# Kernel optimization log

Measured on AMD Instinct MI355X. Metric: run time of the kernel, lower is better.

## Reference

```python
import jax, jax.numpy as jnp
import numpy as np

K = 2            # num_classes (fixed in module)
THRESH = 0.01    # CdistThreshold
MAX_ITERS = 3    # loop breaks when Ci > 3 -> at most 3 work iterations


def _l2norm(x, eps=1e-12):
    # torch F.normalize(dim=1) on [N, C]-style rows -> normalize last axis here
    n = jnp.linalg.norm(x, axis=-1, keepdims=True)
    return x / jnp.maximum(n, eps)


def _step(feats, centers):
    """One k-means iteration, vectorized over batch.
    feats:   [B, N, C]  centers: [K, C]
    Returns (new_centers [K,C], CurDist scalar, labels [B,N])."""
    B = feats.shape[0]
    fn = _l2norm(feats)
    cn = _l2norm(centers)
    # cosine distance 0.5*(1 - cos_sim): [B, N, K]
    dists = 0.5 * (1.0 - jnp.einsum('bnc,kc->bnk', fn, cn))
    labels = jnp.argmin(dists, axis=-1)                      # [B, N]
    mask = jax.nn.one_hot(labels, K, dtype=feats.dtype)      # [B, N, K]
    sums = jnp.einsum('bnc,bnk->bkc', feats, mask)           # [B, K, C]
    counts = jnp.sum(mask, axis=1)                           # [B, K]
    centers_iter = sums / (counts[..., None] + 1.0)          # [B, K, C] (note +1 as in torch)
    # per-batch mean cosine similarity between new per-batch centers and old centers
    num = jnp.sum(centers_iter * centers[None], axis=-1)     # [B, K]
    den = jnp.maximum(
        jnp.linalg.norm(centers_iter, axis=-1) * jnp.linalg.norm(centers, axis=-1)[None],
        1e-8)
    cdist = jnp.mean(num / den, axis=-1)                     # [B]
    new_centers = jnp.sum(centers_iter, axis=0) / B          # centersIterout / B
    cur_dist = jnp.sum(cdist) / B                            # CdistT / B
    return new_centers, cur_dist, labels


def setup_inputs() -> dict:
    key = jax.random.key(0)
    k1, k2 = jax.random.split(key)
    FeatureT = jax.random.normal(k1, (8, 256, 256, 256), dtype=jnp.float32)
    centerInit = jax.random.normal(k2, (K, 256), dtype=jnp.float32)
    return {"FeatureT": FeatureT, "centerInit": centerInit}


def reference(FeatureT, centerInit):
    B, C = FeatureT.shape[0], FeatureT.shape[1]
    feats = FeatureT.reshape(B, C, -1).transpose(0, 2, 1)    # [B, N, C]
    # iteration 1 always runs (centers = centerInit)
    centers, cur_dist, labels = _step(feats, centerInit)
    done = cur_dist < THRESH
    # iterations 2..3, frozen once converged (matches the while-loop break)
    for _ in range(MAX_ITERS - 1):
        nc, cd, lb = _step(feats, centers)
        centers = jnp.where(done, centers, nc)
        labels = jnp.where(done, labels, lb)
        cur_dist = jnp.where(done, cur_dist, cd)
        done = done | (cur_dist < THRESH)
    labels_onehot = jax.nn.one_hot(labels.reshape(-1), K, dtype=jnp.float32)  # [B*N, K]
    # torch returns centersIterout.detach()
    return jax.lax.stop_gradient(centers), labels, labels_onehot, cur_dist
```

## Files before the change

### kernel.cpp

```cpp
#include <hip/hip_runtime.h>
#include <stdint.h>

#define CDIM   256
#define NPIX   65536
#define NBATCH 8
#define SLABS  64
#define SCOLS  1024
#define NBLOCKS (NBATCH * SLABS)
#define KTHRESH 0.01

#define WS_DELTA 0
#define WS_CENT  256
#define WS_T     768
#define WS_S1    2816
#define WS_CNT   4864
#define WS_DONE  4872

#define OUT_LABELS 512
#define OUT_ONEHOT (512 + NBATCH * NPIX)
#define OUT_CDIST  (512 + NBATCH * NPIX + 2 * NBATCH * NPIX)

__device__ __forceinline__ double block_reduce(double v, double* sh) {
  const int t = threadIdx.x;
  #pragma unroll
  for (int off = 32; off > 0; off >>= 1) v += __shfl_down(v, off, 64);
  __syncthreads();
  if ((t & 63) == 0) sh[t >> 6] = v;
  __syncthreads();
  return sh[0] + sh[1] + sh[2] + sh[3];
}

__device__ __forceinline__ void block_reduce4(double v[4], double* sh) {
  const int t = threadIdx.x;
  #pragma unroll
  for (int off = 32; off > 0; off >>= 1) {
    v[0] += __shfl_down(v[0], off, 64);
    v[1] += __shfl_down(v[1], off, 64);
    v[2] += __shfl_down(v[2], off, 64);
    v[3] += __shfl_down(v[3], off, 64);
  }
  __syncthreads();
  if ((t & 63) == 0) {
    const int w = t >> 6;
    sh[w] = v[0]; sh[4 + w] = v[1]; sh[8 + w] = v[2]; sh[12 + w] = v[3];
  }
  __syncthreads();
  #pragma unroll
  for (int k = 0; k < 4; ++k) v[k] = sh[4 * k] + sh[4 * k + 1] + sh[4 * k + 2] + sh[4 * k + 3];
}

__global__ __launch_bounds__(256) void init_kernel(const float* __restrict__ cinit,
                                                   float* __restrict__ ws) {
  __shared__ double sh[16];
  const int t = threadIdx.x;
  for (int i = t; i < NBATCH * CDIM; i += 256) { ws[WS_T + i] = 0.f; ws[WS_S1 + i] = 0.f; }
  if (t < NBATCH) ((unsigned int*)(ws + WS_CNT))[t] = 0u;
  if (t == 0) ((int*)(ws + WS_DONE))[0] = 0;
  const float c0f = cinit[t], c1f = cinit[CDIM + t];
  ws[WS_CENT + t] = c0f;
  ws[WS_CENT + CDIM + t] = c1f;
  const double c0 = (double)c0f, c1 = (double)c1f;
  double n0 = sqrt(block_reduce(c0 * c0, sh));
  double n1 = sqrt(block_reduce(c1 * c1, sh));
  n0 = fmax(n0, 1e-12); n1 = fmax(n1, 1e-12);
  ws[WS_DELTA + t] = (float)(c1 / n1) - (float)(c0 / n0);
}

__global__ __launch_bounds__(256) void pass_kernel(const float* __restrict__ F,
                                                   float* __restrict__ ws,
                                                   float* __restrict__ out,
                                                   int iter) {
  if (iter > 0 && ((const volatile int*)(ws + WS_DONE))[0] != 0) return;

  __shared__ double deltaD[CDIM];
  __shared__ float s1p[CDIM * 4];
  __shared__ float tp[CDIM * 4];
  __shared__ unsigned cntS;

  const int t = threadIdx.x;
  const int w = t >> 6;
  const int l = t & 63;
  const int b = blockIdx.x >> 6;
  const int n0 = (blockIdx.x & 63) * SCOLS;

  if (t < CDIM) deltaD[t] = (double)ws[WS_DELTA + t];
  if (t == 0) cntS = 0u;
  __syncthreads();

  const float4* __restrict__ Fv =
      (const float4*)(F + (size_t)b * CDIM * NPIX + n0);
  const int rstride = NPIX / 4;

  double d0 = 0.0, d1 = 0.0, d2 = 0.0, d3 = 0.0;
  #pragma unroll 16
  for (int c = 0; c < CDIM; ++c) {
    const float4 v = Fv[(size_t)c * rstride + t];
    const double dc = deltaD[c];
    d0 = fma(dc, (double)v.x, d0);
    d1 = fma(dc, (double)v.y, d1);
    d2 = fma(dc, (double)v.z, d2);
    d3 = fma(dc, (double)v.w, d3);
  }
  const float m0 = d0 > 0.0 ? 1.f : 0.f;
  const float m1 = d1 > 0.0 ? 1.f : 0.f;
  const float m2 = d2 > 0.0 ? 1.f : 0.f;
  const float m3 = d3 > 0.0 ? 1.f : 0.f;

  const int gi0 = b * NPIX + n0 + 4 * t;
  *(float4*)(out + OUT_LABELS + gi0) = make_float4(m0, m1, m2, m3);
  *(float4*)(out + OUT_ONEHOT + 2 * gi0)     = make_float4(1.f - m0, m0, 1.f - m1, m1);
  *(float4*)(out + OUT_ONEHOT + 2 * gi0 + 4) = make_float4(1.f - m2, m2, 1.f - m3, m3);

  const unsigned cw = (unsigned)(__popcll(__ballot(d0 > 0.0)) +
                                 __popcll(__ballot(d1 > 0.0)) +
                                 __popcll(__ballot(d2 > 0.0)) +
                                 __popcll(__ballot(d3 > 0.0)));
  if (l == 0) atomicAdd(&cntS, cw);

  const bool first = (iter == 0);
  #pragma unroll 8
  for (int c = CDIM - 1; c >= 0; --c) {
    const float4 v = Fv[(size_t)c * rstride + t];
    float s1 = 0.f;
    s1 = fmaf(m0, v.x, s1);
    s1 = fmaf(m1, v.y, s1);
    s1 = fmaf(m2, v.z, s1);
    s1 = fmaf(m3, v.w, s1);
    #pragma unroll
    for (int off = 32; off > 0; off >>= 1) s1 += __shfl_down(s1, off, 64);
    if (l == 0) s1p[4 * c + w] = s1;
    if (first) {
      float tc = (v.x + v.y) + (v.z + v.w);
      #pragma unroll
      for (int off = 32; off > 0; off >>= 1) tc += __shfl_down(tc, off, 64);
      if (l == 0) tp[4 * c + w] = tc;
    }
  }
  __syncthreads();

  {
    const float s = (s1p[4 * t] + s1p[4 * t + 1]) + (s1p[4 * t + 2] + s1p[4 * t + 3]);
    unsafeAtomicAdd(&ws[WS_S1 + b * CDIM + t], s);
    if (first) {
      const float tt = (tp[4 * t] + tp[4 * t + 1]) + (tp[4 * t + 2] + tp[4 * t + 3]);
      unsafeAtomicAdd(&ws[WS_T + b * CDIM + t], tt);
    }
  }
  if (t == 0) atomicAdd(&((unsigned int*)(ws + WS_CNT))[b], cntS);
}

__global__ __launch_bounds__(256) void finalize_kernel(float* __restrict__ ws,
                                                       float* __restrict__ out) {
  __shared__ double sh[16];
  const int t = threadIdx.x;
  if (((const volatile int*)(ws + WS_DONE))[0] != 0) return;

  const double cold0 = (double)ws[WS_CENT + t];
  const double cold1 = (double)ws[WS_CENT + CDIM + t];
  const double normc0 = sqrt(block_reduce(cold0 * cold0, sh));
  const double normc1 = sqrt(block_reduce(cold1 * cold1, sh));

  double acc0 = 0.0, acc1 = 0.0, cdsum = 0.0;
  for (int b = 0; b < NBATCH; ++b) {
    const double s1v  = (double)ws[WS_S1 + b * CDIM + t];
    const double totv = (double)ws[WS_T  + b * CDIM + t];
    const double c1n  = (double)((unsigned int*)(ws + WS_CNT))[b];
    const double ci1  = s1v / (c1n + 1.0);
    const double ci0  = (totv - s1v) / ((double)NPIX - c1n + 1.0);
    acc0 += ci0; acc1 += ci1;
    double v[4] = {ci0 * cold0, ci0 * ci0, ci1 * cold1, ci1 * ci1};
    block_reduce4(v, sh);
    const double den0 = fmax(sqrt(v[1]) * normc0, 1e-8);
    const double den1 = fmax(sqrt(v[3]) * normc1, 1e-8);
    cdsum += 0.5 * (v[0] / den0 + v[2] / den1);
  }
  const double curdist = cdsum / (double)NBATCH;
  const float nc0f = (float)(acc0 / (double)NBATCH);
  const float nc1f = (float)(acc1 / (double)NBATCH);

  ws[WS_CENT + t] = nc0f;
  ws[WS_CENT + CDIM + t] = nc1f;
  out[t] = nc0f;
  out[CDIM + t] = nc1f;
  if (t == 0) out[OUT_CDIST] = (float)curdist;

  double m0 = sqrt(block_reduce((double)nc0f * (double)nc0f, sh));
  double m1 = sqrt(block_reduce((double)nc1f * (double)nc1f, sh));
  m0 = fmax(m0, 1e-12); m1 = fmax(m1, 1e-12);
  ws[WS_DELTA + t] = (float)((double)nc1f / m1) - (float)((double)nc0f / m0);

  __syncthreads();
  for (int i = t; i < NBATCH * CDIM; i += 256) ws[WS_S1 + i] = 0.f;
  if (t < NBATCH) ((unsigned int*)(ws + WS_CNT))[t] = 0u;
  if (t == 0) ((int*)(ws + WS_DONE))[0] = (curdist < KTHRESH) ? 1 : 0;
}

extern "C" void kernel_launch(void* const* d_in, const int* in_sizes, int n_in,
                              void* d_out, int out_size, void* d_ws, size_t ws_size,
                              hipStream_t stream) {
  const float* F     = (const float*)d_in[0];
  const float* cinit = (const float*)d_in[1];
  float* out = (float*)d_out;
  float* ws  = (float*)d_ws;

  init_kernel<<<1, 256, 0, stream>>>(cinit, ws);
  for (int iter = 0; iter < 3; ++iter) {
    pass_kernel<<<NBLOCKS, 256, 0, stream>>>(F, ws, out, iter);
    finalize_kernel<<<1, 256, 0, stream>>>(ws, out);
  }
}
```

Baseline: 1.396 ms.

## Transpose features to pixel-major once and fuse distance and sum passes

Adds a one-time transpose kernel that copies the channel-major features into a pixel-major workspace and accumulates per-channel totals along the way. Each k-means pass then reads every pixel's 256 channels contiguously, once, and computes both the assignment and the masked sums from registers, instead of streaming the feature tensor twice per iteration. The cost is an extra full read plus write of the feature tensor for the transpose, and a workspace large enough to hold a copy of it.

```diff
diff --git a/kernel.cpp b/kernel.cpp
--- a/kernel.cpp
+++ b/kernel.cpp
@@ -4,9 +4,6 @@
 #define CDIM   256
 #define NPIX   65536
 #define NBATCH 8
-#define SLABS  64
-#define SCOLS  1024
-#define NBLOCKS (NBATCH * SLABS)
 #define KTHRESH 0.01
 
 #define WS_DELTA 0
@@ -15,6 +12,7 @@
 #define WS_S1    2816
 #define WS_CNT   4864
 #define WS_DONE  4872
+#define WS_FT    8192
 
 #define OUT_LABELS 512
 #define OUT_ONEHOT (512 + NBATCH * NPIX)
@@ -66,86 +64,124 @@
   ws[WS_DELTA + t] = (float)(c1 / n1) - (float)(c0 / n0);
 }
 
-__global__ __launch_bounds__(256) void pass_kernel(const float* __restrict__ F,
-                                                   float* __restrict__ ws,
-                                                   float* __restrict__ out,
-                                                   int iter) {
+__global__ __launch_bounds__(256, 2) void transpose_kernel(const float* __restrict__ F,
+                                                           float* __restrict__ ws) {
+  __shared__ float tile[64 * 257];
+  const int t = threadIdx.x, w = t >> 6, l = t & 63;
+  const int bid  = blockIdx.x;
+  const int b    = bid >> 10;
+  const int cblk = (bid >> 8) & 3;
+  const int nblk = bid & 255;
+  const int c0 = cblk * 64;
+  const size_t n0 = (size_t)nblk * 256;
+
+  const float* Fb = F + ((size_t)b * CDIM + c0) * NPIX + n0;
+
+  #pragma unroll
+  for (int i = 0; i < 16; ++i) {
+    const int r = w * 16 + i;
+    const float4 v = ((const float4*)(Fb + (size_t)r * NPIX))[l];
+    float* rowp = tile + r * 257 + 4 * l;
+    rowp[0] = v.x; rowp[1] = v.y; rowp[2] = v.z; rowp[3] = v.w;
+    float p = (v.x + v.y) + (v.z + v.w);
+    #pragma unroll
+    for (int off = 32; off > 0; off >>= 1) p += __shfl_down(p, off, 64);
+    if (l == 0) unsafeAtomicAdd(&ws[WS_T + b * CDIM + c0 + r], p);
+  }
+  __syncthreads();
+
+  float* FTp = ws + WS_FT + ((size_t)b * NPIX + n0) * CDIM + c0;
+  #pragma unroll 8
+  for (int i = 0; i < 64; ++i) {
+    const int n = w * 64 + i;
+    FTp[(size_t)n * CDIM + l] = tile[l * 257 + n];
+  }
+}
+
+__global__ __launch_bounds__(256, 4) void pass_kernel(float* __restrict__ ws,
+                                                      float* __restrict__ out,
+                                                      int iter) {
   if (iter > 0 && ((const volatile int*)(ws + WS_DONE))[0] != 0) return;
 
-  __shared__ double deltaD[CDIM];
-  __shared__ float s1p[CDIM * 4];
-  __shared__ float tp[CDIM * 4];
+  __shared__ float deltaS[CDIM];
+  __shared__ float s1sh[4 * CDIM];
   __shared__ unsigned cntS;
 
-  const int t = threadIdx.x;
-  const int w = t >> 6;
-  const int l = t & 63;
-  const int b = blockIdx.x >> 6;
-  const int n0 = (blockIdx.x & 63) * SCOLS;
-
-  if (t < CDIM) deltaD[t] = (double)ws[WS_DELTA + t];
+  const int t = threadIdx.x, w = t >> 6, l = t & 63;
+  const int o  = l & 7;
+  const int cq = l >> 3;
+  const int b  = blockIdx.x >> 8;
+  const int n0 = (blockIdx.x & 255) * 256;
+
+  deltaS[t] = ws[WS_DELTA + t];
   if (t == 0) cntS = 0u;
   __syncthreads();
 
-  const float4* __restrict__ Fv =
-      (const float4*)(F + (size_t)b * CDIM * NPIX + n0);
-  const int rstride = NPIX / 4;
-
-  double d0 = 0.0, d1 = 0.0, d2 = 0.0, d3 = 0.0;
-  #pragma unroll 16
-  for (int c = 0; c < CDIM; ++c) {
-    const float4 v = Fv[(size_t)c * rstride + t];
-    const double dc = deltaD[c];
-    d0 = fma(dc, (double)v.x, d0);
-    d1 = fma(dc, (double)v.y, d1);
-    d2 = fma(dc, (double)v.z, d2);
-    d3 = fma(dc, (double)v.w, d3);
-  }
-  const float m0 = d0 > 0.0 ? 1.f : 0.f;
-  const float m1 = d1 > 0.0 ? 1.f : 0.f;
-  const float m2 = d2 > 0.0 ? 1.f : 0.f;
-  const float m3 = d3 > 0.0 ? 1.f : 0.f;
-
-  const int gi0 = b * NPIX + n0 + 4 * t;
-  *(float4*)(out + OUT_LABELS + gi0) = make_float4(m0, m1, m2, m3);
-  *(float4*)(out + OUT_ONEHOT + 2 * gi0)     = make_float4(1.f - m0, m0, 1.f - m1, m1);
-  *(float4*)(out + OUT_ONEHOT + 2 * gi0 + 4) = make_float4(1.f - m2, m2, 1.f - m3, m3);
-
-  const unsigned cw = (unsigned)(__popcll(__ballot(d0 > 0.0)) +
-                                 __popcll(__ballot(d1 > 0.0)) +
-                                 __popcll(__ballot(d2 > 0.0)) +
-                                 __popcll(__ballot(d3 > 0.0)));
-  if (l == 0) atomicAdd(&cntS, cw);
-
-  const bool first = (iter == 0);
-  #pragma unroll 8
-  for (int c = CDIM - 1; c >= 0; --c) {
-    const float4 v = Fv[(size_t)c * rstride + t];
-    float s1 = 0.f;
-    s1 = fmaf(m0, v.x, s1);
-    s1 = fmaf(m1, v.y, s1);
-    s1 = fmaf(m2, v.z, s1);
-    s1 = fmaf(m3, v.w, s1);
-    #pragma unroll
-    for (int off = 32; off > 0; off >>= 1) s1 += __shfl_down(s1, off, 64);
-    if (l == 0) s1p[4 * c + w] = s1;
-    if (first) {
-      float tc = (v.x + v.y) + (v.z + v.w);
-      #pragma unroll
-      for (int off = 32; off > 0; off >>= 1) tc += __shfl_down(tc, off, 64);
-      if (l == 0) tp[4 * c + w] = tc;
-    }
-  }
-  __syncthreads();
-
-  {
-    const float s = (s1p[4 * t] + s1p[4 * t + 1]) + (s1p[4 * t + 2] + s1p[4 * t + 3]);
-    unsafeAtomicAdd(&ws[WS_S1 + b * CDIM + t], s);
-    if (first) {
-      const float tt = (tp[4 * t] + tp[4 * t + 1]) + (tp[4 * t + 2] + tp[4 * t + 3]);
-      unsafeAtomicAdd(&ws[WS_T + b * CDIM + t], tt);
-    }
-  }
+  const float* FTb = ws + WS_FT + (size_t)b * NPIX * CDIM;
+
+  float4 macc[8];
+  #pragma unroll
+  for (int j = 0; j < 8; ++j) macc[j] = make_float4(0.f, 0.f, 0.f, 0.f);
+  unsigned cnt = 0;
+
+  for (int g = 0; g < 8; ++g) {
+    const int n = n0 + g * 32 + w * 8 + cq;
+    const float4* colp = (const float4*)(FTb + (size_t)n * CDIM);
+    float4 v[8];
+    #pragma unroll
+    for (int j = 0; j < 8; ++j) v[j] = colp[8 * j + o];
+
+    double d = 0.0;
+    #pragma unroll
+    for (int j = 0; j < 8; ++j) {
+      const float4 dl = ((const float4*)deltaS)[8 * j + o];
+      d = fma((double)dl.x, (double)v[j].x, d);
+      d = fma((double)dl.y, (double)v[j].y, d);
+      d = fma((double)dl.z, (double)v[j].z, d);
+      d = fma((double)dl.w, (double)v[j].w, d);
+    }
+    d += __shfl_xor(d, 1, 64);
+    d += __shfl_xor(d, 2, 64);
+    d += __shfl_xor(d, 4, 64);
+
+    const unsigned long long ball = __ballot(d > 0.0);
+    cnt += (unsigned)__popcll(ball & 0x0101010101010101ull);
+
+    const float m = d > 0.0 ? 1.f : 0.f;
+    if (o == 0) {
+      const int gi = b * NPIX + n;
+      out[OUT_LABELS + gi] = m;
+      ((float2*)(out + OUT_ONEHOT))[gi] = make_float2(1.f - m, m);
+    }
+    #pragma unroll
+    for (int j = 0; j < 8; ++j) {
+      macc[j].x = fmaf(m, v[j].x, macc[j].x);
+      macc[j].y = fmaf(m, v[j].y, macc[j].y);
+      macc[j].z = fmaf(m, v[j].z, macc[j].z);
+      macc[j].w = fmaf(m, v[j].w, macc[j].w);
+    }
+  }
+
+  #pragma unroll
+  for (int s = 8; s < 64; s <<= 1) {
+    #pragma unroll
+    for (int j = 0; j < 8; ++j) {
+      macc[j].x += __shfl_xor(macc[j].x, s, 64);
+      macc[j].y += __shfl_xor(macc[j].y, s, 64);
+      macc[j].z += __shfl_xor(macc[j].z, s, 64);
+      macc[j].w += __shfl_xor(macc[j].w, s, 64);
+    }
+  }
+  if (l < 8) {
+    #pragma unroll
+    for (int j = 0; j < 8; ++j)
+      ((float4*)(s1sh + w * CDIM))[8 * j + l] = macc[j];
+  }
+  if (l == 0) atomicAdd(&cntS, cnt);
+  __syncthreads();
+
+  const float s = (s1sh[t] + s1sh[CDIM + t]) + (s1sh[2 * CDIM + t] + s1sh[3 * CDIM + t]);
+  unsafeAtomicAdd(&ws[WS_S1 + b * CDIM + t], s);
   if (t == 0) atomicAdd(&((unsigned int*)(ws + WS_CNT))[b], cntS);
 }
 
@@ -204,8 +240,9 @@
   float* ws  = (float*)d_ws;
 
   init_kernel<<<1, 256, 0, stream>>>(cinit, ws);
+  transpose_kernel<<<NBATCH * 4 * 256, 256, 0, stream>>>(F, ws);
   for (int iter = 0; iter < 3; ++iter) {
-    pass_kernel<<<NBLOCKS, 256, 0, stream>>>(F, ws, out, iter);
+    pass_kernel<<<NBATCH * 256, 256, 0, stream>>>(ws, out, iter);
     finalize_kernel<<<1, 256, 0, stream>>>(ws, out);
   }
 }
```

Result: slower. 1.718 ms (+23.1%).

## Retile pass kernel to 256-pixel blocks with transposed per-thread channel reduction

Applied to the files above, without the earlier changes.

The pass kernel now gives each block 256 pixels (one per thread) and launches 2048 blocks instead of 512. It batches 32 channel loads per thread for the distance dot product. The second sweep is transposed so each thread owns one channel and reads a contiguous row of 256 pixels, with labels staged in shared memory. This replaces the per-channel wave shuffle reductions and shared partial arrays with plain per-thread accumulation, at the cost of scalar loads in the first sweep and four times as many global atomics. The finalize kernel is also parallelised across 8 waves, one per batch, in place of a serial loop over batches with block reductions.

```diff
diff --git a/kernel.cpp b/kernel.cpp
--- a/kernel.cpp
+++ b/kernel.cpp
@@ -4,9 +4,6 @@
 #define CDIM   256
 #define NPIX   65536
 #define NBATCH 8
-#define SLABS  64
-#define SCOLS  1024
-#define NBLOCKS (NBATCH * SLABS)
 #define KTHRESH 0.01
 
 #define WS_DELTA 0
@@ -30,23 +27,10 @@
   return sh[0] + sh[1] + sh[2] + sh[3];
 }
 
-__device__ __forceinline__ void block_reduce4(double v[4], double* sh) {
-  const int t = threadIdx.x;
-  #pragma unroll
-  for (int off = 32; off > 0; off >>= 1) {
-    v[0] += __shfl_down(v[0], off, 64);
-    v[1] += __shfl_down(v[1], off, 64);
-    v[2] += __shfl_down(v[2], off, 64);
-    v[3] += __shfl_down(v[3], off, 64);
-  }
-  __syncthreads();
-  if ((t & 63) == 0) {
-    const int w = t >> 6;
-    sh[w] = v[0]; sh[4 + w] = v[1]; sh[8 + w] = v[2]; sh[12 + w] = v[3];
-  }
-  __syncthreads();
-  #pragma unroll
-  for (int k = 0; k < 4; ++k) v[k] = sh[4 * k] + sh[4 * k + 1] + sh[4 * k + 2] + sh[4 * k + 3];
+__device__ __forceinline__ double wave_reduce(double v) {
+  #pragma unroll
+  for (int off = 32; off > 0; off >>= 1) v += __shfl_xor(v, off, 64);
+  return v;
 }
 
 __global__ __launch_bounds__(256) void init_kernel(const float* __restrict__ cinit,
@@ -66,131 +50,153 @@
   ws[WS_DELTA + t] = (float)(c1 / n1) - (float)(c0 / n0);
 }
 
-__global__ __launch_bounds__(256) void pass_kernel(const float* __restrict__ F,
-                                                   float* __restrict__ ws,
-                                                   float* __restrict__ out,
-                                                   int iter) {
+__global__ __launch_bounds__(256, 4) void pass_kernel(const float* __restrict__ F,
+                                                      float* __restrict__ ws,
+                                                      float* __restrict__ out,
+                                                      int iter) {
   if (iter > 0 && ((const volatile int*)(ws + WS_DONE))[0] != 0) return;
 
   __shared__ double deltaD[CDIM];
-  __shared__ float s1p[CDIM * 4];
-  __shared__ float tp[CDIM * 4];
+  __shared__ float mlab[CDIM];
   __shared__ unsigned cntS;
 
-  const int t = threadIdx.x;
-  const int w = t >> 6;
-  const int l = t & 63;
-  const int b = blockIdx.x >> 6;
-  const int n0 = (blockIdx.x & 63) * SCOLS;
-
-  if (t < CDIM) deltaD[t] = (double)ws[WS_DELTA + t];
+  const int t = threadIdx.x, l = t & 63;
+  const int b  = blockIdx.x >> 8;
+  const int n0 = (blockIdx.x & 255) * 256;
+
+  deltaD[t] = (double)ws[WS_DELTA + t];
   if (t == 0) cntS = 0u;
   __syncthreads();
 
-  const float4* __restrict__ Fv =
-      (const float4*)(F + (size_t)b * CDIM * NPIX + n0);
-  const int rstride = NPIX / 4;
-
-  double d0 = 0.0, d1 = 0.0, d2 = 0.0, d3 = 0.0;
-  #pragma unroll 16
-  for (int c = 0; c < CDIM; ++c) {
-    const float4 v = Fv[(size_t)c * rstride + t];
-    const double dc = deltaD[c];
-    d0 = fma(dc, (double)v.x, d0);
-    d1 = fma(dc, (double)v.y, d1);
-    d2 = fma(dc, (double)v.z, d2);
-    d3 = fma(dc, (double)v.w, d3);
-  }
-  const float m0 = d0 > 0.0 ? 1.f : 0.f;
-  const float m1 = d1 > 0.0 ? 1.f : 0.f;
-  const float m2 = d2 > 0.0 ? 1.f : 0.f;
-  const float m3 = d3 > 0.0 ? 1.f : 0.f;
-
-  const int gi0 = b * NPIX + n0 + 4 * t;
-  *(float4*)(out + OUT_LABELS + gi0) = make_float4(m0, m1, m2, m3);
-  *(float4*)(out + OUT_ONEHOT + 2 * gi0)     = make_float4(1.f - m0, m0, 1.f - m1, m1);
-  *(float4*)(out + OUT_ONEHOT + 2 * gi0 + 4) = make_float4(1.f - m2, m2, 1.f - m3, m3);
-
-  const unsigned cw = (unsigned)(__popcll(__ballot(d0 > 0.0)) +
-                                 __popcll(__ballot(d1 > 0.0)) +
-                                 __popcll(__ballot(d2 > 0.0)) +
-                                 __popcll(__ballot(d3 > 0.0)));
-  if (l == 0) atomicAdd(&cntS, cw);
-
-  const bool first = (iter == 0);
-  #pragma unroll 8
-  for (int c = CDIM - 1; c >= 0; --c) {
-    const float4 v = Fv[(size_t)c * rstride + t];
-    float s1 = 0.f;
-    s1 = fmaf(m0, v.x, s1);
-    s1 = fmaf(m1, v.y, s1);
-    s1 = fmaf(m2, v.z, s1);
-    s1 = fmaf(m3, v.w, s1);
-    #pragma unroll
-    for (int off = 32; off > 0; off >>= 1) s1 += __shfl_down(s1, off, 64);
-    if (l == 0) s1p[4 * c + w] = s1;
-    if (first) {
-      float tc = (v.x + v.y) + (v.z + v.w);
+  const float* __restrict__ Fb = F + (size_t)b * CDIM * NPIX;
+
+  double a0 = 0.0, a1 = 0.0, a2 = 0.0, a3 = 0.0;
+  {
+    const float* __restrict__ p = Fb + n0 + t;
+    for (int cc = 0; cc < CDIM; cc += 32) {
+      float v[32];
       #pragma unroll
-      for (int off = 32; off > 0; off >>= 1) tc += __shfl_down(tc, off, 64);
-      if (l == 0) tp[4 * c + w] = tc;
+      for (int j = 0; j < 32; ++j) v[j] = p[(size_t)(cc + j) * NPIX];
+      #pragma unroll
+      for (int j = 0; j < 32; j += 4) {
+        a0 = fma(deltaD[cc + j + 0], (double)v[j + 0], a0);
+        a1 = fma(deltaD[cc + j + 1], (double)v[j + 1], a1);
+        a2 = fma(deltaD[cc + j + 2], (double)v[j + 2], a2);
+        a3 = fma(deltaD[cc + j + 3], (double)v[j + 3], a3);
+      }
     }
   }
-  __syncthreads();
-
-  {
-    const float s = (s1p[4 * t] + s1p[4 * t + 1]) + (s1p[4 * t + 2] + s1p[4 * t + 3]);
-    unsafeAtomicAdd(&ws[WS_S1 + b * CDIM + t], s);
-    if (first) {
-      const float tt = (tp[4 * t] + tp[4 * t + 1]) + (tp[4 * t + 2] + tp[4 * t + 3]);
-      unsafeAtomicAdd(&ws[WS_T + b * CDIM + t], tt);
+  const double d = (a0 + a1) + (a2 + a3);
+  const float m = d > 0.0 ? 1.f : 0.f;
+  mlab[t] = m;
+  const unsigned long long ball = __ballot(d > 0.0);
+  if (l == 0) atomicAdd(&cntS, (unsigned)__popcll(ball));
+
+  const int gi = b * NPIX + n0 + t;
+  out[OUT_LABELS + gi] = m;
+  ((float2*)(out + OUT_ONEHOT))[gi] = make_float2(1.f - m, m);
+  __syncthreads();
+
+  float s1 = 0.f, tot = 0.f;
+  const float4* __restrict__ rp = (const float4*)(Fb + (size_t)t * NPIX + n0);
+  const float4* __restrict__ ml4 = (const float4*)mlab;
+  for (int q = 0; q < 64; q += 8) {
+    float4 v[8];
+    #pragma unroll
+    for (int j = 0; j < 8; ++j) v[j] = rp[q + j];
+    #pragma unroll
+    for (int j = 0; j < 8; ++j) {
+      const float4 mm = ml4[q + j];
+      s1 = fmaf(mm.x, v[j].x, s1);
+      s1 = fmaf(mm.y, v[j].y, s1);
+      s1 = fmaf(mm.z, v[j].z, s1);
+      s1 = fmaf(mm.w, v[j].w, s1);
+      tot += (v[j].x + v[j].y) + (v[j].z + v[j].w);
     }
   }
+  unsafeAtomicAdd(&ws[WS_S1 + b * CDIM + t], s1);
+  if (iter == 0) unsafeAtomicAdd(&ws[WS_T + b * CDIM + t], tot);
   if (t == 0) atomicAdd(&((unsigned int*)(ws + WS_CNT))[b], cntS);
 }
 
-__global__ __launch_bounds__(256) void finalize_kernel(float* __restrict__ ws,
+__global__ __launch_bounds__(512) void finalize_kernel(float* __restrict__ ws,
                                                        float* __restrict__ out) {
-  __shared__ double sh[16];
-  const int t = threadIdx.x;
   if (((const volatile int*)(ws + WS_DONE))[0] != 0) return;
 
-  const double cold0 = (double)ws[WS_CENT + t];
-  const double cold1 = (double)ws[WS_CENT + CDIM + t];
-  const double normc0 = sqrt(block_reduce(cold0 * cold0, sh));
-  const double normc1 = sqrt(block_reduce(cold1 * cold1, sh));
-
-  double acc0 = 0.0, acc1 = 0.0, cdsum = 0.0;
-  for (int b = 0; b < NBATCH; ++b) {
-    const double s1v  = (double)ws[WS_S1 + b * CDIM + t];
-    const double totv = (double)ws[WS_T  + b * CDIM + t];
-    const double c1n  = (double)((unsigned int*)(ws + WS_CNT))[b];
-    const double ci1  = s1v / (c1n + 1.0);
-    const double ci0  = (totv - s1v) / ((double)NPIX - c1n + 1.0);
-    acc0 += ci0; acc1 += ci1;
-    double v[4] = {ci0 * cold0, ci0 * ci0, ci1 * cold1, ci1 * ci1};
-    block_reduce4(v, sh);
-    const double den0 = fmax(sqrt(v[1]) * normc0, 1e-8);
-    const double den1 = fmax(sqrt(v[3]) * normc1, 1e-8);
-    cdsum += 0.5 * (v[0] / den0 + v[2] / den1);
-  }
-  const double curdist = cdsum / (double)NBATCH;
-  const float nc0f = (float)(acc0 / (double)NBATCH);
-  const float nc1f = (float)(acc1 / (double)NBATCH);
-
-  ws[WS_CENT + t] = nc0f;
-  ws[WS_CENT + CDIM + t] = nc1f;
-  out[t] = nc0f;
-  out[CDIM + t] = nc1f;
-  if (t == 0) out[OUT_CDIST] = (float)curdist;
-
-  double m0 = sqrt(block_reduce((double)nc0f * (double)nc0f, sh));
-  double m1 = sqrt(block_reduce((double)nc1f * (double)nc1f, sh));
-  m0 = fmax(m0, 1e-12); m1 = fmax(m1, 1e-12);
-  ws[WS_DELTA + t] = (float)((double)nc1f / m1) - (float)((double)nc0f / m0);
-
-  __syncthreads();
-  for (int i = t; i < NBATCH * CDIM; i += 256) ws[WS_S1 + i] = 0.f;
+  __shared__ double ci0sh[NBATCH][CDIM];
+  __shared__ double ci1sh[NBATCH][CDIM];
+  __shared__ double cdsh[NBATCH];
+  __shared__ double sh2[16];
+
+  const int t = threadIdx.x, w = t >> 6, l = t & 63;
+  const int b = w;
+
+  double c0k[4], c1k[4], p0 = 0.0, p1 = 0.0;
+  #pragma unroll
+  for (int k = 0; k < 4; ++k) {
+    const int c = l + 64 * k;
+    c0k[k] = (double)ws[WS_CENT + c];
+    c1k[k] = (double)ws[WS_CENT + CDIM + c];
+    p0 += c0k[k] * c0k[k];
+    p1 += c1k[k] * c1k[k];
+  }
+  const double normc0 = sqrt(wave_reduce(p0));
+  const double normc1 = sqrt(wave_reduce(p1));
+
+  const double c1n = (double)((unsigned int*)(ws + WS_CNT))[b];
+  double v0 = 0.0, v1 = 0.0, v2 = 0.0, v3 = 0.0;
+  #pragma unroll
+  for (int k = 0; k < 4; ++k) {
+    const int c = l + 64 * k;
+    const double s1v  = (double)ws[WS_S1 + b * CDIM + c];
+    const double totv = (double)ws[WS_T  + b * CDIM + c];
+    const double ci1 = s1v / (c1n + 1.0);
+    const double ci0 = (totv - s1v) / ((double)NPIX - c1n + 1.0);
+    ci0sh[b][c] = ci0; ci1sh[b][c] = ci1;
+    v0 += ci0 * c0k[k]; v1 += ci0 * ci0;
+    v2 += ci1 * c1k[k]; v3 += ci1 * ci1;
+  }
+  v0 = wave_reduce(v0); v1 = wave_reduce(v1);
+  v2 = wave_reduce(v2); v3 = wave_reduce(v3);
+  if (l == 0) {
+    const double den0 = fmax(sqrt(v1) * normc0, 1e-8);
+    const double den1 = fmax(sqrt(v3) * normc1, 1e-8);
+    cdsh[b] = 0.5 * (v0 / den0 + v2 / den1);
+  }
+  __syncthreads();
+
+  float nc0f = 0.f, nc1f = 0.f;
+  if (t < CDIM) {
+    double a0 = 0.0, a1 = 0.0;
+    #pragma unroll
+    for (int bb = 0; bb < NBATCH; ++bb) { a0 += ci0sh[bb][t]; a1 += ci1sh[bb][t]; }
+    nc0f = (float)(a0 / (double)NBATCH);
+    nc1f = (float)(a1 / (double)NBATCH);
+    ws[WS_CENT + t] = nc0f;
+    ws[WS_CENT + CDIM + t] = nc1f;
+    out[t] = nc0f; out[CDIM + t] = nc1f;
+  }
+  double curdist = 0.0;
+  if (t == 0) {
+    #pragma unroll
+    for (int bb = 0; bb < NBATCH; ++bb) curdist += cdsh[bb];
+    curdist /= (double)NBATCH;
+    out[OUT_CDIST] = (float)curdist;
+  }
+
+  double q0 = (t < CDIM) ? (double)nc0f * (double)nc0f : 0.0;
+  double q1 = (t < CDIM) ? (double)nc1f * (double)nc1f : 0.0;
+  q0 = wave_reduce(q0); q1 = wave_reduce(q1);
+  if (l == 0) { sh2[w] = q0; sh2[8 + w] = q1; }
+  __syncthreads();
+  double m0 = 0.0, m1 = 0.0;
+  #pragma unroll
+  for (int k = 0; k < 8; ++k) { m0 += sh2[k]; m1 += sh2[8 + k]; }
+  m0 = fmax(sqrt(m0), 1e-12); m1 = fmax(sqrt(m1), 1e-12);
+  if (t < CDIM)
+    ws[WS_DELTA + t] = (float)((double)nc1f / m1) - (float)((double)nc0f / m0);
+
+  for (int i = t; i < NBATCH * CDIM; i += 512) ws[WS_S1 + i] = 0.f;
   if (t < NBATCH) ((unsigned int*)(ws + WS_CNT))[t] = 0u;
   if (t == 0) ((int*)(ws + WS_DONE))[0] = (curdist < KTHRESH) ? 1 : 0;
 }
@@ -205,7 +211,7 @@
 
   init_kernel<<<1, 256, 0, stream>>>(cinit, ws);
   for (int iter = 0; iter < 3; ++iter) {
-    pass_kernel<<<NBLOCKS, 256, 0, stream>>>(F, ws, out, iter);
-    finalize_kernel<<<1, 256, 0, stream>>>(ws, out);
-  }
-}
+    pass_kernel<<<NBATCH * 256, 256, 0, stream>>>(F, ws, out, iter);
+    finalize_kernel<<<1, 512, 0, stream>>>(ws, out);
+  }
+}
```

Result: no change. 1.395 ms (-0.0%).
